# Kernel optimization log

Measured on AMD Instinct MI355X. Metric: run time of the kernel, lower is better.

## Reference

```python
import jax, jax.numpy as jnp
import numpy as np

N = 50000
E = 800000
IN_C = 128
HID = 16
HEADS = 8
OUT_C = 64
NEG_SLOPE = 0.2


def setup_inputs() -> dict:
    key = jax.random.key(0)
    ks = jax.random.split(key, 12)
    x = jax.random.normal(ks[0], (N, IN_C), dtype=jnp.float32)
    edge_index = jax.random.randint(ks[1], (2, E), 0, N, dtype=jnp.int32)
    s = 0.1
    W1 = jax.random.normal(ks[2], (IN_C, HEADS * HID), dtype=jnp.float32) * s
    a1_src = jax.random.normal(ks[3], (HEADS, HID), dtype=jnp.float32) * s
    a1_dst = jax.random.normal(ks[4], (HEADS, HID), dtype=jnp.float32) * s
    b1 = jnp.zeros((HEADS * HID,), dtype=jnp.float32)
    W2 = jax.random.normal(ks[5], (HEADS * HID, OUT_C), dtype=jnp.float32) * s
    a2_src = jax.random.normal(ks[6], (1, OUT_C), dtype=jnp.float32) * s
    a2_dst = jax.random.normal(ks[7], (1, OUT_C), dtype=jnp.float32) * s
    b2 = jnp.zeros((OUT_C,), dtype=jnp.float32)
    return {"x": x, "edge_index": edge_index, "W1": W1, "a1_src": a1_src,
            "a1_dst": a1_dst, "b1": b1, "W2": W2, "a2_src": a2_src,
            "a2_dst": a2_dst, "b2": b2}


def gat_conv(x, src, dst, W, a_src, a_dst, b, heads, ch):
    # linear projection -> [N, H, C]
    h = (x @ W).reshape(N, heads, ch)
    # per-node attention logits [N, H]
    al_s = jnp.einsum('nhc,hc->nh', h, a_src)
    al_d = jnp.einsum('nhc,hc->nh', h, a_dst)
    # per-edge logits [E, H]
    e = jax.nn.leaky_relu(al_s[src] + al_d[dst], NEG_SLOPE)
    # segment softmax over incoming edges of each dst node
    emax = jax.ops.segment_max(e, dst, num_segments=N)
    ee = jnp.exp(e - emax[dst])
    denom = jax.ops.segment_sum(ee, dst, num_segments=N)
    alpha = ee / (denom[dst] + 1e-16)
    # weighted scatter-aggregate of source messages
    msg = h[src] * alpha[:, :, None]  # [E, H, C]
    out = jax.ops.segment_sum(msg, dst, num_segments=N)
    return out.reshape(N, heads * ch) + b


def reference(x, edge_index, W1, a1_src, a1_dst, b1, W2, a2_src, a2_dst, b2):
    # add self loops (PyG GATConv default add_self_loops=True)
    loops = jnp.arange(N, dtype=edge_index.dtype)
    src = jnp.concatenate([edge_index[0], loops])
    dst = jnp.concatenate([edge_index[1], loops])
    h = gat_conv(x, src, dst, W1, a1_src, a1_dst, b1, HEADS, HID)
    h = jax.nn.relu(h)
    # dropout p=0.6 is identity in eval mode
    out = gat_conv(h, src, dst, W2, a2_src, a2_dst, b2, 1, OUT_C)
    return out
```

## Files before the change

### kernel.cpp

```cpp
#include <hip/hip_runtime.h>
#include <hip/hip_fp16.h>
#include <math.h>

#define N_NODES 50000
#define E_EDGES 800000
#define IN_C    128
#define HID     16
#define HEADS   8
#define OUT_C   64
#define NEG_SLOPE 0.2f
#define CELLW   64

typedef _Float16 half8 __attribute__((ext_vector_type(8)));
typedef _Float16 half4 __attribute__((ext_vector_type(4)));
typedef float floatx4 __attribute__((ext_vector_type(4)));

__device__ __forceinline__ float lrelu_exp(float v) {
    v = v > 0.f ? v : NEG_SLOPE * v;
    return __expf(v);
}

__device__ __forceinline__ void gload_lds16(const void* g, void* l) {
    __builtin_amdgcn_global_load_lds(
        (const __attribute__((address_space(1))) void*)g,
        (__attribute__((address_space(3))) void*)l, 16, 0, 0);
}

__global__ __launch_bounds__(256) void prep(
    const float* __restrict__ W1, _Float16* __restrict__ W1t, int* __restrict__ cursor) {
    const int t = threadIdx.x;
    const int n = blockIdx.x * 256 + t;
    if (n < N_NODES) cursor[n] = 0;
    if (blockIdx.x == 0) {
        const int col = t & 127;
        const int kq = (t >> 7) * 4;
        for (int it = 0; it < 16; ++it) {
            const int k0 = it * 8 + kq;
            half4 hv;
            hv[0] = (_Float16)W1[(size_t)(k0 + 0) * IN_C + col];
            hv[1] = (_Float16)W1[(size_t)(k0 + 1) * IN_C + col];
            hv[2] = (_Float16)W1[(size_t)(k0 + 2) * IN_C + col];
            hv[3] = (_Float16)W1[(size_t)(k0 + 3) * IN_C + col];
            *(half4*)&W1t[col * 136 + k0] = hv;
        }
    }
}

__global__ __launch_bounds__(256) void fused_gemm_fill(
    const float* __restrict__ X, const _Float16* __restrict__ W1t, __half* __restrict__ H,
    const float* __restrict__ a_src, const float* __restrict__ a_dst,
    float* __restrict__ als, float* __restrict__ ald,
    const int* __restrict__ src, const int* __restrict__ dst,
    int* __restrict__ cursor, int* __restrict__ ell) {
    __shared__ _Float16 wT[IN_C * 136];
    const int bid = blockIdx.x;
    const int t = threadIdx.x;

    if (bid & 1) {
        const int tid = (bid >> 1) * 256 + t;
        if (tid < E_EDGES / 4) {
            const int4 s4 = ((const int4*)src)[tid];
            const int4 d4 = ((const int4*)dst)[tid];
            const int p0 = atomicAdd(&cursor[d4.x], 1);
            const int p1 = atomicAdd(&cursor[d4.y], 1);
            const int p2 = atomicAdd(&cursor[d4.z], 1);
            const int p3 = atomicAdd(&cursor[d4.w], 1);
            if (p0 < CELLW) __builtin_nontemporal_store(s4.x, &ell[(size_t)d4.x * CELLW + p0]);
            if (p1 < CELLW) __builtin_nontemporal_store(s4.y, &ell[(size_t)d4.y * CELLW + p1]);
            if (p2 < CELLW) __builtin_nontemporal_store(s4.z, &ell[(size_t)d4.z * CELLW + p2]);
            if (p3 < CELLW) __builtin_nontemporal_store(s4.w, &ell[(size_t)d4.w * CELLW + p3]);
        }
        return;
    }

    {
        const char* g = (const char*)W1t;
        char* l = (char*)wT;
        const int o = t * 16;
#pragma unroll
        for (int it = 0; it < 8; ++it) {
            const int off = it * 4096 + o;
            gload_lds16(g + off, l + off);
        }
        if (t < 128) {
            const int off = 32768 + o;
            gload_lds16(g + off, l + off);
        }
    }

    const int wave = t >> 6, lane = t & 63;
    const int m = lane & 15, quad = lane >> 4;
    const int r0w = (bid >> 1) * 64 + wave * 16;
    int rl = r0w + m;
    if (rl >= N_NODES) rl = N_NODES - 1;
    const float* Xr = X + (size_t)rl * IN_C;

    float4 xv[8];
#pragma unroll
    for (int kc = 0; kc < 4; ++kc) {
        const int k8 = kc * 32 + quad * 8;
        xv[kc * 2]     = *(const float4*)(Xr + k8);
        xv[kc * 2 + 1] = *(const float4*)(Xr + k8 + 4);
    }

    __syncthreads();

    floatx4 acc[8];
#pragma unroll
    for (int i = 0; i < 8; ++i) acc[i] = (floatx4){0.f, 0.f, 0.f, 0.f};

#pragma unroll
    for (int kc = 0; kc < 4; ++kc) {
        const int k8 = kc * 32 + quad * 8;
        const float4 xa = xv[kc * 2];
        const float4 xb = xv[kc * 2 + 1];
        half8 a;
        a[0] = (_Float16)xa.x; a[1] = (_Float16)xa.y;
        a[2] = (_Float16)xa.z; a[3] = (_Float16)xa.w;
        a[4] = (_Float16)xb.x; a[5] = (_Float16)xb.y;
        a[6] = (_Float16)xb.z; a[7] = (_Float16)xb.w;
#pragma unroll
        for (int ct = 0; ct < 8; ++ct) {
            const half8 b = *(const half8*)&wT[(ct * 16 + m) * 136 + k8];
            acc[ct] = __builtin_amdgcn_mfma_f32_16x16x32_f16(a, b, acc[ct], 0, 0, 0);
        }
    }

    _Float16* Hh = (_Float16*)H;
#pragma unroll
    for (int ct = 0; ct < 8; ++ct) {
        const float asv = a_src[ct * 16 + m];
        const float adv = a_dst[ct * 16 + m];
#pragma unroll
        for (int r = 0; r < 4; ++r) {
            const int row = r0w + quad * 4 + r;
            const float c = acc[ct][r];
            float ps = c * asv, pd = c * adv;
            ps += __shfl_xor(ps, 1); pd += __shfl_xor(pd, 1);
            ps += __shfl_xor(ps, 2); pd += __shfl_xor(pd, 2);
            ps += __shfl_xor(ps, 4); pd += __shfl_xor(pd, 4);
            ps += __shfl_xor(ps, 8); pd += __shfl_xor(pd, 8);
            if (row < N_NODES) {
                Hh[(size_t)row * IN_C + ct * 16 + m] = (_Float16)c;
                if (m == 0) {
                    als[(size_t)row * HEADS + ct] = ps;
                    ald[(size_t)row * HEADS + ct] = pd;
                }
            }
        }
    }
}

__global__ __launch_bounds__(256) void agg1_gemm2(
    const int* __restrict__ cnt, const int* __restrict__ ell,
    const float* __restrict__ als, const float* __restrict__ ald,
    const __half* __restrict__ H, const float* __restrict__ b,
    const float* __restrict__ W2, const float* __restrict__ a2_src,
    const float* __restrict__ a2_dst, __half* __restrict__ H2,
    float* __restrict__ als2, float* __restrict__ ald2) {
    __shared__ _Float16 w2T[OUT_C * 136];
    __shared__ _Float16 xrowh[32 * 136];
    __shared__ float l2buf[2][32][2];
    const int t = threadIdx.x;

    {
        const int col = t & 63;
        const int kg = t >> 6;
        for (int k0 = kg * 32; k0 < kg * 32 + 32; k0 += 4) {
            half4 hv;
            hv[0] = (_Float16)W2[(size_t)(k0 + 0) * OUT_C + col];
            hv[1] = (_Float16)W2[(size_t)(k0 + 1) * OUT_C + col];
            hv[2] = (_Float16)W2[(size_t)(k0 + 2) * OUT_C + col];
            hv[3] = (_Float16)W2[(size_t)(k0 + 3) * OUT_C + col];
            *(half4*)&w2T[col * 136 + k0] = hv;
        }
    }

    const int nl = t >> 3, h = t & 7;
    int nc = blockIdx.x * 32 + nl;
    if (nc >= N_NODES) nc = N_NODES - 1;
    int deg = cnt[nc];
    deg = deg < CELLW ? deg : CELLW;
    const int* ep = ell + (size_t)nc * CELLW;
    const float ad = ald[nc * HEADS + h];
    float accv[16];
    float ssum;
    {
        const float w = lrelu_exp(als[nc * HEADS + h] + ad);
        const half8* q = (const half8*)(H + ((size_t)nc * HEADS + h) * HID);
        const half8 u0 = q[0], u1 = q[1];
        ssum = w;
#pragma unroll
        for (int j = 0; j < 8; ++j) {
            accv[j] = w * (float)u0[j];
            accv[j + 8] = w * (float)u1[j];
        }
    }
    for (int p = 0; p < deg; p += 4) {
        const int4 s4 = *(const int4*)(ep + p);
        const int s0 = s4.x;
        const int i1 = (p + 1 < deg) ? s4.y : nc;
        const int i2 = (p + 2 < deg) ? s4.z : nc;
        const int i3 = (p + 3 < deg) ? s4.w : nc;
        const float f1 = (p + 1 < deg) ? 1.f : 0.f;
        const float f2 = (p + 2 < deg) ? 1.f : 0.f;
        const float f3 = (p + 3 < deg) ? 1.f : 0.f;
        const float v0 = als[s0 * HEADS + h];
        const float v1 = als[i1 * HEADS + h];
        const float v2 = als[i2 * HEADS + h];
        const float v3 = als[i3 * HEADS + h];
        const half8* q0 = (const half8*)(H + ((size_t)s0 * HEADS + h) * HID);
        const half8* q1 = (const half8*)(H + ((size_t)i1 * HEADS + h) * HID);
        const half8* q2 = (const half8*)(H + ((size_t)i2 * HEADS + h) * HID);
        const half8* q3 = (const half8*)(H + ((size_t)i3 * HEADS + h) * HID);
        const half8 a0 = q0[0], b0 = q0[1];
        const half8 a1 = q1[0], b1 = q1[1];
        const half8 a2 = q2[0], b2 = q2[1];
        const half8 a3 = q3[0], b3 = q3[1];
        const float w0 = lrelu_exp(v0 + ad);
        const float w1 = lrelu_exp(v1 + ad) * f1;
        const float w2 = lrelu_exp(v2 + ad) * f2;
        const float w3 = lrelu_exp(v3 + ad) * f3;
        ssum += (w0 + w1) + (w2 + w3);
#pragma unroll
        for (int j = 0; j < 8; ++j) {
            accv[j]     += w0 * (float)a0[j] + w1 * (float)a1[j] +
                           w2 * (float)a2[j] + w3 * (float)a3[j];
            accv[j + 8] += w0 * (float)b0[j] + w1 * (float)b1[j] +
                           w2 * (float)b2[j] + w3 * (float)b3[j];
        }
    }
    {
        const float inv = 1.f / (ssum + 1e-16f);
        half8 r0, r1;
#pragma unroll
        for (int j = 0; j < 8; ++j) {
            float ra = accv[j] * inv + b[h * 16 + j];
            float rb = accv[j + 8] * inv + b[h * 16 + 8 + j];
            r0[j] = (_Float16)(ra > 0.f ? ra : 0.f);
            r1[j] = (_Float16)(rb > 0.f ? rb : 0.f);
        }
        _Float16* xr = &xrowh[nl * 136 + h * 16];
        *(half8*)(xr) = r0;
        *(half8*)(xr + 8) = r1;
    }

    __syncthreads();

    {
        const int wv = t >> 6, ln = t & 63;
        const int bm = ln & 15, quad = ln >> 4;
        const int mt = wv >> 1;
        const int ntg = wv & 1;
        floatx4 acc0 = (floatx4){0.f, 0.f, 0.f, 0.f};
        floatx4 acc1 = (floatx4){0.f, 0.f, 0.f, 0.f};
        const _Float16* arow  = &xrowh[(mt * 16 + bm) * 136];
        const _Float16* brow0 = &w2T[(ntg * 32 + bm) * 136];
        const _Float16* brow1 = &w2T[(ntg * 32 + 16 + bm) * 136];
#pragma unroll
        for (int kc = 0; kc < 4; ++kc) {
            const int k8 = kc * 32 + quad * 8;
            const half8 a   = *(const half8*)(arow + k8);
            const half8 b0v = *(const half8*)(brow0 + k8);
            const half8 b1v = *(const half8*)(brow1 + k8);
            acc0 = __builtin_amdgcn_mfma_f32_16x16x32_f16(a, b0v, acc0, 0, 0, 0);
            acc1 = __builtin_amdgcn_mfma_f32_16x16x32_f16(a, b1v, acc1, 0, 0, 0);
        }
        const float a2s0 = a2_src[ntg * 32 + bm],      a2d0 = a2_dst[ntg * 32 + bm];
        const float a2s1 = a2_src[ntg * 32 + 16 + bm], a2d1 = a2_dst[ntg * 32 + 16 + bm];
        _Float16* H2h = (_Float16*)H2;
        float psr[4], pdr[4];
#pragma unroll
        for (int r = 0; r < 4; ++r) {
            const float c0 = acc0[r], c1 = acc1[r];
            float ps = c0 * a2s0 + c1 * a2s1;
            float pd = c0 * a2d0 + c1 * a2d1;
            ps += __shfl_xor(ps, 1); pd += __shfl_xor(pd, 1);
            ps += __shfl_xor(ps, 2); pd += __shfl_xor(pd, 2);
            ps += __shfl_xor(ps, 4); pd += __shfl_xor(pd, 4);
            ps += __shfl_xor(ps, 8); pd += __shfl_xor(pd, 8);
            psr[r] = ps; pdr[r] = pd;
            const int row = blockIdx.x * 32 + mt * 16 + quad * 4 + r;
            if (row < N_NODES) {
                H2h[(size_t)row * OUT_C + ntg * 32 + bm] = (_Float16)c0;
                H2h[(size_t)row * OUT_C + ntg * 32 + 16 + bm] = (_Float16)c1;
            }
        }
        if (bm == 0) {
#pragma unroll
            for (int r = 0; r < 4; ++r) {
                l2buf[ntg][mt * 16 + quad * 4 + r][0] = psr[r];
                l2buf[ntg][mt * 16 + quad * 4 + r][1] = pdr[r];
            }
        }
    }
    __syncthreads();
    if (t < 32) {
        const int n2 = blockIdx.x * 32 + t;
        if (n2 < N_NODES) {
            als2[n2] = l2buf[0][t][0] + l2buf[1][t][0];
            ald2[n2] = l2buf[0][t][1] + l2buf[1][t][1];
        }
    }
}

__global__ __launch_bounds__(256) void agg2(
    const int* __restrict__ cnt, const int* __restrict__ ell,
    const float* __restrict__ als, const float* __restrict__ ald,
    const __half* __restrict__ H, const float* __restrict__ b,
    float* __restrict__ out) {
    const int t = threadIdx.x;
    int n = blockIdx.x * 32 + (t >> 3);
    const int j0 = (t & 7) * 8;
    const bool valid = n < N_NODES;
    if (!valid) n = N_NODES - 1;
    int deg = cnt[n];
    deg = deg < CELLW ? deg : CELLW;
    const int* ep = ell + (size_t)n * CELLW;
    const float ad = ald[n];
    float accv[8];
    float ssum;
    {
        const float w = lrelu_exp(als[n] + ad);
        const half8 u = *(const half8*)(H + (size_t)n * OUT_C + j0);
        ssum = w;
#pragma unroll
        for (int k = 0; k < 8; ++k) accv[k] = w * (float)u[k];
    }
    for (int p = 0; p < deg; p += 4) {
        const int4 s4 = *(const int4*)(ep + p);
        const int s0 = s4.x;
        const int i1 = (p + 1 < deg) ? s4.y : n;
        const int i2 = (p + 2 < deg) ? s4.z : n;
        const int i3 = (p + 3 < deg) ? s4.w : n;
        const float f1 = (p + 1 < deg) ? 1.f : 0.f;
        const float f2 = (p + 2 < deg) ? 1.f : 0.f;
        const float f3 = (p + 3 < deg) ? 1.f : 0.f;
        const float v0 = als[s0];
        const float v1 = als[i1];
        const float v2 = als[i2];
        const float v3 = als[i3];
        const half8 u0 = *(const half8*)(H + (size_t)s0 * OUT_C + j0);
        const half8 u1 = *(const half8*)(H + (size_t)i1 * OUT_C + j0);
        const half8 u2 = *(const half8*)(H + (size_t)i2 * OUT_C + j0);
        const half8 u3 = *(const half8*)(H + (size_t)i3 * OUT_C + j0);
        const float w0 = lrelu_exp(v0 + ad);
        const float w1 = lrelu_exp(v1 + ad) * f1;
        const float w2 = lrelu_exp(v2 + ad) * f2;
        const float w3 = lrelu_exp(v3 + ad) * f3;
        ssum += (w0 + w1) + (w2 + w3);
#pragma unroll
        for (int k = 0; k < 8; ++k)
            accv[k] += w0 * (float)u0[k] + w1 * (float)u1[k] +
                       w2 * (float)u2[k] + w3 * (float)u3[k];
    }
    if (valid) {
        const float inv = 1.f / (ssum + 1e-16f);
        floatx4 r0, r1;
        r0[0] = accv[0] * inv + b[j0 + 0]; r0[1] = accv[1] * inv + b[j0 + 1];
        r0[2] = accv[2] * inv + b[j0 + 2]; r0[3] = accv[3] * inv + b[j0 + 3];
        r1[0] = accv[4] * inv + b[j0 + 4]; r1[1] = accv[5] * inv + b[j0 + 5];
        r1[2] = accv[6] * inv + b[j0 + 6]; r1[3] = accv[7] * inv + b[j0 + 7];
        float* op = out + (size_t)n * OUT_C + j0;
        __builtin_nontemporal_store(r0, (floatx4*)op);
        __builtin_nontemporal_store(r1, (floatx4*)(op + 4));
    }
}

extern "C" void kernel_launch(void* const* d_in, const int* in_sizes, int n_in,
                              void* d_out, int out_size, void* d_ws, size_t ws_size,
                              hipStream_t stream) {
    const float* x      = (const float*)d_in[0];
    const int*   ei     = (const int*)d_in[1];
    const float* W1     = (const float*)d_in[2];
    const float* a1_src = (const float*)d_in[3];
    const float* a1_dst = (const float*)d_in[4];
    const float* b1     = (const float*)d_in[5];
    const float* W2     = (const float*)d_in[6];
    const float* a2_src = (const float*)d_in[7];
    const float* a2_dst = (const float*)d_in[8];
    const float* b2     = (const float*)d_in[9];
    const int* src = ei;
    const int* dst = ei + E_EDGES;
    float* outp = (float*)d_out;

    char* wsb = (char*)d_ws;
    __half* h1   = (__half*)wsb;
    __half* h2   = h1 + (size_t)N_NODES * IN_C;
    float*  als1 = (float*)(h2 + (size_t)N_NODES * OUT_C);
    float*  ald1 = als1 + N_NODES * HEADS;
    float*  als2 = ald1 + N_NODES * HEADS;
    float*  ald2 = als2 + N_NODES;
    int*    cursor = (int*)(ald2 + N_NODES);
    int*    ell    = cursor + N_NODES;

    _Float16* W1t = (_Float16*)als2;

    prep<<<(N_NODES + 255) / 256, 256, 0, stream>>>(W1, W1t, cursor);

    {
        const int gemm_blocks = (N_NODES + 63) / 64;
        fused_gemm_fill<<<gemm_blocks * 2, 256, 0, stream>>>(
            x, W1t, h1, a1_src, a1_dst, als1, ald1, src, dst, cursor, ell);
    }

    agg1_gemm2<<<(N_NODES + 31) / 32, 256, 0, stream>>>(
        cursor, ell, als1, ald1, h1, b1, W2, a2_src, a2_dst, h2, als2, ald2);

    agg2<<<(N_NODES + 31) / 32, 256, 0, stream>>>(
        cursor, ell, als2, ald2, h2, b2, outp);
}
```

Before: 192.3 us.

## Fold attention vectors into GEMM weights and co-schedule ELL fill in same block

Precomputes W1·a_src and W1·a_dst as 16 extra fp16 weight columns, so the attention logits come out of a ninth MFMA tile instead of per-row shuffle reductions. Merges the GEMM and ELL-fill roles into one 512-thread block, 4 waves each, instead of alternating blocks, sharing the LDS weight load. Only half of X is preloaded before the barrier to cut register pressure. In exchange, the logits are computed from fp16-rounded folded weights, which may lose accuracy, the weight tile grows to 144 columns, and a 512-thread block occupies more LDS.

Result: slower. 210.3 us (+9.4%).

```diff
diff --git a/kernel.cpp b/kernel.cpp
--- a/kernel.cpp
+++ b/kernel.cpp
@@ -11,6 +11,10 @@
 #define NEG_SLOPE 0.2f
 #define CELLW   64
 
+#define WCOLS   144
+#define WSTRIDE 136
+#define WBYTES  (WCOLS * WSTRIDE * 2)
+
 typedef _Float16 half8 __attribute__((ext_vector_type(8)));
 typedef _Float16 half4 __attribute__((ext_vector_type(4)));
 typedef float floatx4 __attribute__((ext_vector_type(4)));
@@ -27,7 +31,9 @@
 }
 
 __global__ __launch_bounds__(256) void prep(
-    const float* __restrict__ W1, _Float16* __restrict__ W1t, int* __restrict__ cursor) {
+    const float* __restrict__ W1, const float* __restrict__ a1_src,
+    const float* __restrict__ a1_dst, _Float16* __restrict__ W1t,
+    int* __restrict__ cursor) {
     const int t = threadIdx.x;
     const int n = blockIdx.x * 256 + t;
     if (n < N_NODES) cursor[n] = 0;
@@ -41,23 +47,69 @@
             hv[1] = (_Float16)W1[(size_t)(k0 + 1) * IN_C + col];
             hv[2] = (_Float16)W1[(size_t)(k0 + 2) * IN_C + col];
             hv[3] = (_Float16)W1[(size_t)(k0 + 3) * IN_C + col];
-            *(half4*)&W1t[col * 136 + k0] = hv;
-        }
-    }
-}
-
-__global__ __launch_bounds__(256) void fused_gemm_fill(
-    const float* __restrict__ X, const _Float16* __restrict__ W1t, __half* __restrict__ H,
-    const float* __restrict__ a_src, const float* __restrict__ a_dst,
+            *(half4*)&W1t[col * WSTRIDE + k0] = hv;
+        }
+    } else if (blockIdx.x == 1) {
+        const int j = t & 15;
+        const int k0 = (t >> 4) * 8;
+        const float* av = (j < 8) ? (a1_src + j * 16) : (a1_dst + (j - 8) * 16);
+        const int hc = (j & 7) * 16;
+        for (int k = k0; k < k0 + 8; ++k) {
+            float s = 0.f;
+#pragma unroll
+            for (int c = 0; c < 16; ++c) s += W1[(size_t)k * IN_C + hc + c] * av[c];
+            W1t[(128 + j) * WSTRIDE + k] = (_Float16)s;
+        }
+    }
+}
+
+__global__ __launch_bounds__(512, 6) void fused_gemm_fill(
+    const float* __restrict__ X, const _Float16* __restrict__ W1t,
+    __half* __restrict__ H,
     float* __restrict__ als, float* __restrict__ ald,
     const int* __restrict__ src, const int* __restrict__ dst,
     int* __restrict__ cursor, int* __restrict__ ell) {
-    __shared__ _Float16 wT[IN_C * 136];
+    __shared__ _Float16 wT[WCOLS * WSTRIDE];
     const int bid = blockIdx.x;
     const int t = threadIdx.x;
 
-    if (bid & 1) {
-        const int tid = (bid >> 1) * 256 + t;
+    {
+        const char* g = (const char*)W1t;
+        char* l = (char*)wT;
+        const int o = t * 16;
+#pragma unroll
+        for (int it = 0; it < 4; ++it) {
+            const int off = it * 8192 + o;
+            gload_lds16(g + off, l + off);
+        }
+        if (t < 400) {
+            const int off = 32768 + o;
+            gload_lds16(g + off, l + off);
+        }
+    }
+
+    const int wave = t >> 6, lane = t & 63;
+    const int m = lane & 15, quad = lane >> 4;
+
+    const float* Xr = nullptr;
+    int r0w = 0;
+    float4 xv0, xv1, xv2, xv3;
+    if (wave < 4) {
+        r0w = bid * 64 + wave * 16;
+        int rl = r0w + m;
+        if (rl >= N_NODES) rl = N_NODES - 1;
+        Xr = X + (size_t)rl * IN_C;
+        const int q8 = quad * 8;
+        xv0 = *(const float4*)(Xr + q8);
+        xv1 = *(const float4*)(Xr + q8 + 4);
+        xv2 = *(const float4*)(Xr + 32 + q8);
+        xv3 = *(const float4*)(Xr + 32 + q8 + 4);
+    }
+
+    __syncthreads();
+
+    if (wave >= 4) {
+        const int tid = bid * 256 + (t - 256);
         if (tid < E_EDGES / 4) {
             const int4 s4 = ((const int4*)src)[tid];
             const int4 d4 = ((const int4*)dst)[tid];
@@ -73,55 +125,28 @@
         return;
     }
 
-    {
-        const char* g = (const char*)W1t;
-        char* l = (char*)wT;
-        const int o = t * 16;
-#pragma unroll
-        for (int it = 0; it < 8; ++it) {
-            const int off = it * 4096 + o;
-            gload_lds16(g + off, l + off);
-        }
-        if (t < 128) {
-            const int off = 32768 + o;
-            gload_lds16(g + off, l + off);
-        }
-    }
-
-    const int wave = t >> 6, lane = t & 63;
-    const int m = lane & 15, quad = lane >> 4;
-    const int r0w = (bid >> 1) * 64 + wave * 16;
-    int rl = r0w + m;
-    if (rl >= N_NODES) rl = N_NODES - 1;
-    const float* Xr = X + (size_t)rl * IN_C;
-
-    float4 xv[8];
+    floatx4 acc[9];
+#pragma unroll
+    for (int i = 0; i < 9; ++i) acc[i] = (floatx4){0.f, 0.f, 0.f, 0.f};
+
 #pragma unroll
     for (int kc = 0; kc < 4; ++kc) {
         const int k8 = kc * 32 + quad * 8;
-        xv[kc * 2]     = *(const float4*)(Xr + k8);
-        xv[kc * 2 + 1] = *(const float4*)(Xr + k8 + 4);
-    }
-
-    __syncthreads();
-
-    floatx4 acc[8];
-#pragma unroll
-    for (int i = 0; i < 8; ++i) acc[i] = (floatx4){0.f, 0.f, 0.f, 0.f};
-
-#pragma unroll
-    for (int kc = 0; kc < 4; ++kc) {
-        const int k8 = kc * 32 + quad * 8;
-        const float4 xa = xv[kc * 2];
-        const float4 xb = xv[kc * 2 + 1];
+        float4 xa, xb;
+        if (kc == 0)      { xa = xv0; xb = xv1; }
+        else if (kc == 1) { xa = xv2; xb = xv3; }
+        else {
+            xa = *(const float4*)(Xr + k8);
+            xb = *(const float4*)(Xr + k8 + 4);
+        }
         half8 a;
         a[0] = (_Float16)xa.x; a[1] = (_Float16)xa.y;
         a[2] = (_Float16)xa.z; a[3] = (_Float16)xa.w;
         a[4] = (_Float16)xb.x; a[5] = (_Float16)xb.y;
         a[6] = (_Float16)xb.z; a[7] = (_Float16)xb.w;
 #pragma unroll
-        for (int ct = 0; ct < 8; ++ct) {
-            const half8 b = *(const half8*)&wT[(ct * 16 + m) * 136 + k8];
+        for (int ct = 0; ct < 9; ++ct) {
+            const half8 b = *(const half8*)&wT[(ct * 16 + m) * WSTRIDE + k8];
             acc[ct] = __builtin_amdgcn_mfma_f32_16x16x32_f16(a, b, acc[ct], 0, 0, 0);
         }
     }
@@ -129,24 +154,19 @@
     _Float16* Hh = (_Float16*)H;
 #pragma unroll
     for (int ct = 0; ct < 8; ++ct) {
-        const float asv = a_src[ct * 16 + m];
-        const float adv = a_dst[ct * 16 + m];
 #pragma unroll
         for (int r = 0; r < 4; ++r) {
             const int row = r0w + quad * 4 + r;
-            const float c = acc[ct][r];
-            float ps = c * asv, pd = c * adv;
-            ps += __shfl_xor(ps, 1); pd += __shfl_xor(pd, 1);
-            ps += __shfl_xor(ps, 2); pd += __shfl_xor(pd, 2);
-            ps += __shfl_xor(ps, 4); pd += __shfl_xor(pd, 4);
-            ps += __shfl_xor(ps, 8); pd += __shfl_xor(pd, 8);
-            if (row < N_NODES) {
-                Hh[(size_t)row * IN_C + ct * 16 + m] = (_Float16)c;
-                if (m == 0) {
-                    als[(size_t)row * HEADS + ct] = ps;
-                    ald[(size_t)row * HEADS + ct] = pd;
-                }
-            }
+            if (row < N_NODES)
+                Hh[(size_t)row * IN_C + ct * 16 + m] = (_Float16)acc[ct][r];
+        }
+    }
+#pragma unroll
+    for (int r = 0; r < 4; ++r) {
+        const int row = r0w + quad * 4 + r;
+        if (row < N_NODES) {
+            if (m < 8) als[(size_t)row * HEADS + m] = acc[8][r];
+            else       ald[(size_t)row * HEADS + (m - 8)] = acc[8][r];
         }
     }
 }
@@ -396,13 +416,10 @@
 
     _Float16* W1t = (_Float16*)als2;
 
-    prep<<<(N_NODES + 255) / 256, 256, 0, stream>>>(W1, W1t, cursor);
-
-    {
-        const int gemm_blocks = (N_NODES + 63) / 64;
-        fused_gemm_fill<<<gemm_blocks * 2, 256, 0, stream>>>(
-            x, W1t, h1, a1_src, a1_dst, als1, ald1, src, dst, cursor, ell);
-    }
+    prep<<<(N_NODES + 255) / 256, 256, 0, stream>>>(W1, a1_src, a1_dst, W1t, cursor);
+
+    fused_gemm_fill<<<(N_NODES + 63) / 64, 512, 0, stream>>>(
+        x, W1t, h1, als1, ald1, src, dst, cursor, ell);
 
     agg1_gemm2<<<(N_NODES + 31) / 32, 256, 0, stream>>>(
         cursor, ell, als1, ald1, h1, b1, W2, a2_src, a2_dst, h2, als2, ald2);
```
